# Optimization experiments

Measured on AMD Instinct MI355X. Metric: run time of the kernel, lower is better.

The kernel has to match this reference:

```python
import jax, jax.numpy as jnp
import numpy as np

B, IN, OUT, NUM_F = 131072, 128, 128, 8


def setup_inputs() -> dict:
    key = jax.random.key(0)
    ks = jax.random.split(key, 6)
    x = jax.random.normal(ks[0], (B, IN), dtype=jnp.float32)
    grid = jnp.arange(NUM_F, dtype=jnp.float32) + 1.0            # nn.Parameter(arange(num_f)+1)
    base_weight = jax.random.normal(ks[1], (OUT, IN), dtype=jnp.float32) * 0.05
    scale_sp = jnp.ones((OUT,), dtype=jnp.float32)
    coef = jax.random.uniform(ks[2], (IN, NUM_F), dtype=jnp.float32)  # torch.rand
    # Conv1d(in=IN*NUM_F, out=OUT*NUM_F, k=1, groups=NUM_F) == per-frequency [OUT, IN] matmul
    fan_in = IN  # per-group in-channels * kernel_size(1)
    bound = 1.0 / np.sqrt(fan_in)
    conv_w = jax.random.uniform(ks[3], (NUM_F, OUT, IN), dtype=jnp.float32,
                                minval=-bound, maxval=bound)
    conv_b = jax.random.uniform(ks[4], (NUM_F, OUT), dtype=jnp.float32,
                                minval=-bound, maxval=bound)
    return {"x": x, "grid": grid, "base_weight": base_weight,
            "scale_sp": scale_sp, "coef": coef, "conv_w": conv_w, "conv_b": conv_b}


def reference(x, grid, base_weight, scale_sp, coef, conv_w, conv_b):
    # base path: SiLU(x) @ W_base^T  -> [B, OUT]
    base_out = jax.nn.silu(x) @ base_weight.T
    # Fourier basis: sin(grid_f * x_i) -> [B, F, I]
    s = jnp.sin(x[:, None, :] * grid[None, :, None])
    # coef [I, F] broadcast-multiplied per (i, f)
    s = s * coef.T[None, :, :]                      # [B, F, I]
    # grouped 1x1 conv == per-frequency matmul, plus per-(f, o) bias
    spline = jnp.einsum('bfi,foi->bfo', s, conv_w) + conv_b[None, :, :]  # [B, F, OUT]
    spline_out = spline.sum(axis=1) * scale_sp      # [B, OUT]
    return base_out + spline_out
```

## Files before the change

### kernel.cpp

```cpp
#include <hip/hip_runtime.h>
#include <stdint.h>

#define NCHUNK 9
#define IN_DIM 128
#define OUT_DIM 128
#define NUM_F 8
#define B_TOTAL 131072

#define WBASE_ELEMS (OUT_DIM * IN_DIM)
#define WSIN_ELEMS (8 * OUT_DIM * IN_DIM)
#define SG_SLICE 32768

typedef __bf16 bf16x8 __attribute__((ext_vector_type(8)));
typedef float floatx16 __attribute__((ext_vector_type(16)));

typedef __attribute__((address_space(1))) const unsigned int gas_u32;
typedef __attribute__((address_space(3))) unsigned int las_u32;

__device__ __forceinline__ unsigned short f2bf_rn(float f) {
  unsigned u = __builtin_bit_cast(unsigned, f);
  u += 0x7FFFu + ((u >> 16) & 1u);
  return (unsigned short)(u >> 16);
}

__global__ void skan_prep(const float* __restrict__ base_w,
                          const float* __restrict__ scale_sp,
                          const float* __restrict__ coef,
                          const float* __restrict__ conv_w,
                          const float* __restrict__ conv_b,
                          unsigned short* __restrict__ Wbase,
                          unsigned short* __restrict__ Wsin,
                          float* __restrict__ bias) {
  int b = blockIdx.x;
  int i = threadIdx.x;
  int j = i & 7, q2 = (i >> 3) & 1;
  if (b < NCHUNK * OUT_DIM) {
    int c = b >> 7;
    int o = b & 127;
    if (c == 0) {
      float v = base_w[o * IN_DIM + i];
      int s = i >> 4;
      Wbase[(s * 2 + q2) * 1024 + o * 8 + j] = f2bf_rn(v);
    } else {
      int f = c - 1;
      float v = conv_w[(f * OUT_DIM + o) * IN_DIM + i] * coef[i * NUM_F + f] * scale_sp[o];
      int sg = i >> 5, s2 = (i >> 4) & 1;
      Wsin[((sg * 8 + f) * 4 + s2 * 2 + q2) * 1024 + o * 8 + j] = f2bf_rn(v);
    }
  } else {
    float s = 0.f;
#pragma unroll
    for (int f = 0; f < NUM_F; ++f) s += conv_b[f * OUT_DIM + i];
    bias[i] = s * scale_sp[i];
  }
}

__device__ __forceinline__ unsigned pack2(float lo, float hi) {
  unsigned ulo = __builtin_bit_cast(unsigned, lo) + 0x8000u;
  unsigned uhi = __builtin_bit_cast(unsigned, hi) + 0x8000u;
  return __builtin_amdgcn_perm(uhi, ulo, 0x07060302u);
}

__device__ __forceinline__ bf16x8 pack_frag(const float* v) {
  union { unsigned u[4]; bf16x8 f; } r;
  r.u[0] = pack2(v[0], v[1]);
  r.u[1] = pack2(v[2], v[3]);
  r.u[2] = pack2(v[4], v[5]);
  r.u[3] = pack2(v[6], v[7]);
  return r.f;
}

__device__ __forceinline__ float silu(float v) {
  return v * __builtin_amdgcn_rcpf(1.f + __expf(-v));
}

__global__ __launch_bounds__(256, 2)
void skan_main(const float* __restrict__ x,
               const unsigned short* __restrict__ Wbase,
               const unsigned short* __restrict__ Wsin,
               const float* __restrict__ bias,
               float* __restrict__ out) {
  __shared__ unsigned short sB[SG_SLICE];

  const int tid  = threadIdx.x;
  const int lane = tid & 63;
  const int w    = tid >> 6;
  const int m    = lane & 31;
  const int q2   = lane >> 5;
  const int rowBase = blockIdx.x * 256 + w * 64;

  const int fragCol = m * 8;

  floatx16 acc[2][4];
#pragma unroll
  for (int mt = 0; mt < 2; ++mt)
#pragma unroll
    for (int nt = 0; nt < 4; ++nt)
#pragma unroll
      for (int e = 0; e < 16; ++e) acc[mt][nt][e] = 0.f;

  const float* xr0 = x + (size_t)(rowBase + m) * IN_DIM;
  const float* xr1 = xr0 + 32 * IN_DIM;

#pragma unroll 1
  for (int sg = 0; sg < 4; ++sg) {
    {
      const char* src = (const char*)(Wsin + sg * SG_SLICE);
      char* dst = (char*)sB;
      int off = tid * 16;
#pragma unroll
      for (int it = 0; it < 16; ++it) {
        __builtin_amdgcn_global_load_lds((gas_u32*)(src + off), (las_u32*)(dst + off),
                                         16, 0, 0);
        off += 4096;
      }
    }

    float xv[2][2][8];
#pragma unroll
    for (int mt = 0; mt < 2; ++mt) {
      const float* xr = mt ? xr1 : xr0;
#pragma unroll
      for (int s2 = 0; s2 < 2; ++s2) {
        float4 a = *(const float4*)(xr + sg * 32 + s2 * 16 + q2 * 8);
        float4 b = *(const float4*)(xr + sg * 32 + s2 * 16 + q2 * 8 + 4);
        xv[mt][s2][0] = a.x; xv[mt][s2][1] = a.y;
        xv[mt][s2][2] = a.z; xv[mt][s2][3] = a.w;
        xv[mt][s2][4] = b.x; xv[mt][s2][5] = b.y;
        xv[mt][s2][6] = b.z; xv[mt][s2][7] = b.w;
      }
    }

#pragma unroll
    for (int s2 = 0; s2 < 2; ++s2) {
      int4 Bb[4];
#pragma unroll
      for (int nt = 0; nt < 4; ++nt)
        Bb[nt] = *(const int4*)(Wbase + ((sg * 2 + s2) * 2 + q2) * 1024 +
                                nt * 256 + fragCol);
      float sv[16];
#pragma unroll
      for (int mt = 0; mt < 2; ++mt)
#pragma unroll
        for (int j = 0; j < 8; ++j) sv[mt * 8 + j] = silu(xv[mt][s2][j]);
      bf16x8 a0 = pack_frag(&sv[0]);
      bf16x8 a1 = pack_frag(&sv[8]);
#pragma unroll
      for (int nt = 0; nt < 4; ++nt) {
        bf16x8 bf = __builtin_bit_cast(bf16x8, Bb[nt]);
        acc[0][nt] = __builtin_amdgcn_mfma_f32_32x32x16_bf16(a0, bf, acc[0][nt], 0, 0, 0);
        acc[1][nt] = __builtin_amdgcn_mfma_f32_32x32x16_bf16(a1, bf, acc[1][nt], 0, 0, 0);
      }
    }

    __syncthreads();

#pragma unroll
    for (int s2 = 0; s2 < 2; ++s2) {
      float sp[16], spp[16], c2[16];
#pragma unroll
      for (int mt = 0; mt < 2; ++mt)
#pragma unroll
        for (int j = 0; j < 8; ++j) {
          int v = mt * 8 + j;
          float xx = xv[mt][s2][j];
          sp[v]  = __sinf(xx);
          c2[v]  = 2.f * __cosf(xx);
          spp[v] = 0.f;
        }

#pragma unroll
      for (int c = 1; c <= 8; ++c) {
        bf16x8 Bf[4];
        const unsigned short* bp = sB + ((c - 1) * 4 + s2 * 2 + q2) * 1024 + fragCol;
#pragma unroll
        for (int nt = 0; nt < 4; ++nt)
          Bf[nt] = *(const bf16x8*)(bp + nt * 256);

        if (c >= 2) {
#pragma unroll
          for (int v = 0; v < 16; ++v) {
            float t = __builtin_fmaf(c2[v], sp[v], -spp[v]);
            spp[v] = sp[v];
            sp[v] = t;
          }
        }
        bf16x8 a0 = pack_frag(&sp[0]);
        bf16x8 a1 = pack_frag(&sp[8]);
#pragma unroll
        for (int nt = 0; nt < 4; ++nt) {
          acc[0][nt] = __builtin_amdgcn_mfma_f32_32x32x16_bf16(a0, Bf[nt], acc[0][nt], 0, 0, 0);
          acc[1][nt] = __builtin_amdgcn_mfma_f32_32x32x16_bf16(a1, Bf[nt], acc[1][nt], 0, 0, 0);
        }
      }
    }

    __syncthreads();
  }

#pragma unroll
  for (int mt = 0; mt < 2; ++mt) {
    float* obase = out + (size_t)(rowBase + mt * 32) * OUT_DIM + m;
#pragma unroll
    for (int nt = 0; nt < 4; ++nt) {
      float bv = bias[nt * 32 + m];
#pragma unroll
      for (int e = 0; e < 16; ++e) {
        int rl = (e & 3) + 8 * (e >> 2) + 4 * q2;
        obase[(size_t)rl * OUT_DIM + nt * 32] = acc[mt][nt][e] + bv;
      }
    }
  }
}

extern "C" void kernel_launch(void* const* d_in, const int* in_sizes, int n_in,
                              void* d_out, int out_size, void* d_ws, size_t ws_size,
                              hipStream_t stream) {
  const float* x      = (const float*)d_in[0];
  const float* base_w = (const float*)d_in[2];
  const float* scale  = (const float*)d_in[3];
  const float* coef   = (const float*)d_in[4];
  const float* conv_w = (const float*)d_in[5];
  const float* conv_b = (const float*)d_in[6];

  unsigned short* Wbase = (unsigned short*)d_ws;
  unsigned short* Wsin  = Wbase + WBASE_ELEMS;
  float* bias = (float*)(Wsin + WSIN_ELEMS);
  float* out  = (float*)d_out;

  skan_prep<<<NCHUNK * OUT_DIM + 1, 128, 0, stream>>>(base_w, scale, coef,
                                                      conv_w, conv_b, Wbase, Wsin, bias);
  skan_main<<<B_TOTAL / 256, 256, 0, stream>>>(x, Wbase, Wsin, bias, out);
}
```

Baseline: 150.4 us.

## Drop LDS staging of sin weights and halve per-wave row tile

Removes the shared-memory staging of the Fourier weight slice and its barriers. Each wave now reads B fragments straight from global memory, relying on L2/L1 caching. Each wave handles 32 rows instead of 64, the grid doubles, and launch bounds rise to 3 blocks per SIMD to improve occupancy. Each weight fragment is now reused across half as many rows, so global/L2 traffic for weights roughly doubles per output row.

```diff
diff --git a/kernel.cpp b/kernel.cpp
--- a/kernel.cpp
+++ b/kernel.cpp
@@ -13,9 +13,6 @@
 
 typedef __bf16 bf16x8 __attribute__((ext_vector_type(8)));
 typedef float floatx16 __attribute__((ext_vector_type(16)));
-
-typedef __attribute__((address_space(1))) const unsigned int gas_u32;
-typedef __attribute__((address_space(3))) unsigned int las_u32;
 
 __device__ __forceinline__ unsigned short f2bf_rn(float f) {
   unsigned u = __builtin_bit_cast(unsigned, f);
@@ -74,61 +71,40 @@
   return v * __builtin_amdgcn_rcpf(1.f + __expf(-v));
 }
 
-__global__ __launch_bounds__(256, 2)
+__global__ __launch_bounds__(256, 3)
 void skan_main(const float* __restrict__ x,
                const unsigned short* __restrict__ Wbase,
                const unsigned short* __restrict__ Wsin,
                const float* __restrict__ bias,
                float* __restrict__ out) {
-  __shared__ unsigned short sB[SG_SLICE];
-
   const int tid  = threadIdx.x;
   const int lane = tid & 63;
   const int w    = tid >> 6;
   const int m    = lane & 31;
   const int q2   = lane >> 5;
-  const int rowBase = blockIdx.x * 256 + w * 64;
+  const int rowBase = blockIdx.x * 128 + w * 32;
 
   const int fragCol = m * 8;
 
-  floatx16 acc[2][4];
+  floatx16 acc[4];
 #pragma unroll
-  for (int mt = 0; mt < 2; ++mt)
+  for (int nt = 0; nt < 4; ++nt)
 #pragma unroll
-    for (int nt = 0; nt < 4; ++nt)
-#pragma unroll
-      for (int e = 0; e < 16; ++e) acc[mt][nt][e] = 0.f;
+    for (int e = 0; e < 16; ++e) acc[nt][e] = 0.f;
 
-  const float* xr0 = x + (size_t)(rowBase + m) * IN_DIM;
-  const float* xr1 = xr0 + 32 * IN_DIM;
+  const float* xr = x + (size_t)(rowBase + m) * IN_DIM;
 
 #pragma unroll 1
   for (int sg = 0; sg < 4; ++sg) {
-    {
-      const char* src = (const char*)(Wsin + sg * SG_SLICE);
-      char* dst = (char*)sB;
-      int off = tid * 16;
+    float xv[2][8];
 #pragma unroll
-      for (int it = 0; it < 16; ++it) {
-        __builtin_amdgcn_global_load_lds((gas_u32*)(src + off), (las_u32*)(dst + off),
-                                         16, 0, 0);
-        off += 4096;
-      }
-    }
-
-    float xv[2][2][8];
-#pragma unroll
-    for (int mt = 0; mt < 2; ++mt) {
-      const float* xr = mt ? xr1 : xr0;
-#pragma unroll
-      for (int s2 = 0; s2 < 2; ++s2) {
-        float4 a = *(const float4*)(xr + sg * 32 + s2 * 16 + q2 * 8);
-        float4 b = *(const float4*)(xr + sg * 32 + s2 * 16 + q2 * 8 + 4);
-        xv[mt][s2][0] = a.x; xv[mt][s2][1] = a.y;
-        xv[mt][s2][2] = a.z; xv[mt][s2][3] = a.w;
-        xv[mt][s2][4] = b.x; xv[mt][s2][5] = b.y;
-        xv[mt][s2][6] = b.z; xv[mt][s2][7] = b.w;
-      }
+    for (int s2 = 0; s2 < 2; ++s2) {
+      float4 a = *(const float4*)(xr + sg * 32 + s2 * 16 + q2 * 8);
+      float4 b = *(const float4*)(xr + sg * 32 + s2 * 16 + q2 * 8 + 4);
+      xv[s2][0] = a.x; xv[s2][1] = a.y;
+      xv[s2][2] = a.z; xv[s2][3] = a.w;
+      xv[s2][4] = b.x; xv[s2][5] = b.y;
+      xv[s2][6] = b.z; xv[s2][7] = b.w;
     }
 
 #pragma unroll
@@ -138,77 +114,61 @@
       for (int nt = 0; nt < 4; ++nt)
         Bb[nt] = *(const int4*)(Wbase + ((sg * 2 + s2) * 2 + q2) * 1024 +
                                 nt * 256 + fragCol);
-      float sv[16];
+      float sv[8];
 #pragma unroll
-      for (int mt = 0; mt < 2; ++mt)
-#pragma unroll
-        for (int j = 0; j < 8; ++j) sv[mt * 8 + j] = silu(xv[mt][s2][j]);
-      bf16x8 a0 = pack_frag(&sv[0]);
-      bf16x8 a1 = pack_frag(&sv[8]);
+      for (int j = 0; j < 8; ++j) sv[j] = silu(xv[s2][j]);
+      bf16x8 a0 = pack_frag(sv);
 #pragma unroll
       for (int nt = 0; nt < 4; ++nt) {
         bf16x8 bf = __builtin_bit_cast(bf16x8, Bb[nt]);
-        acc[0][nt] = __builtin_amdgcn_mfma_f32_32x32x16_bf16(a0, bf, acc[0][nt], 0, 0, 0);
-        acc[1][nt] = __builtin_amdgcn_mfma_f32_32x32x16_bf16(a1, bf, acc[1][nt], 0, 0, 0);
+        acc[nt] = __builtin_amdgcn_mfma_f32_32x32x16_bf16(a0, bf, acc[nt], 0, 0, 0);
       }
     }
 
-    __syncthreads();
-
+    const unsigned short* wsg = Wsin + sg * SG_SLICE;
 #pragma unroll
     for (int s2 = 0; s2 < 2; ++s2) {
-      float sp[16], spp[16], c2[16];
+      float sp[8], spp[8], c2[8];
 #pragma unroll
-      for (int mt = 0; mt < 2; ++mt)
-#pragma unroll
-        for (int j = 0; j < 8; ++j) {
-          int v = mt * 8 + j;
-          float xx = xv[mt][s2][j];
-          sp[v]  = __sinf(xx);
-          c2[v]  = 2.f * __cosf(xx);
-          spp[v] = 0.f;
-        }
+      for (int j = 0; j < 8; ++j) {
+        float xx = xv[s2][j];
+        sp[j]  = __sinf(xx);
+        c2[j]  = 2.f * __cosf(xx);
+        spp[j] = 0.f;
+      }
 
 #pragma unroll
       for (int c = 1; c <= 8; ++c) {
         bf16x8 Bf[4];
-        const unsigned short* bp = sB + ((c - 1) * 4 + s2 * 2 + q2) * 1024 + fragCol;
+        const unsigned short* bp = wsg + ((c - 1) * 4 + s2 * 2 + q2) * 1024 + fragCol;
 #pragma unroll
         for (int nt = 0; nt < 4; ++nt)
           Bf[nt] = *(const bf16x8*)(bp + nt * 256);
 
         if (c >= 2) {
 #pragma unroll
-          for (int v = 0; v < 16; ++v) {
-            float t = __builtin_fmaf(c2[v], sp[v], -spp[v]);
-            spp[v] = sp[v];
-            sp[v] = t;
+          for (int j = 0; j < 8; ++j) {
+            float t = __builtin_fmaf(c2[j], sp[j], -spp[j]);
+            spp[j] = sp[j];
+            sp[j] = t;
           }
         }
-        bf16x8 a0 = pack_frag(&sp[0]);
-        bf16x8 a1 = pack_frag(&sp[8]);
+        bf16x8 a0 = pack_frag(sp);
 #pragma unroll
-        for (int nt = 0; nt < 4; ++nt) {
-          acc[0][nt] = __builtin_amdgcn_mfma_f32_32x32x16_bf16(a0, Bf[nt], acc[0][nt], 0, 0, 0);
-          acc[1][nt] = __builtin_amdgcn_mfma_f32_32x32x16_bf16(a1, Bf[nt], acc[1][nt], 0, 0, 0);
-        }
+        for (int nt = 0; nt < 4; ++nt)
+          acc[nt] = __builtin_amdgcn_mfma_f32_32x32x16_bf16(a0, Bf[nt], acc[nt], 0, 0, 0);
       }
     }
-
-    __syncthreads();
   }
 
+  float* obase = out + (size_t)rowBase * OUT_DIM + m;
 #pragma unroll
-  for (int mt = 0; mt < 2; ++mt) {
-    float* obase = out + (size_t)(rowBase + mt * 32) * OUT_DIM + m;
+  for (int nt = 0; nt < 4; ++nt) {
+    float bv = bias[nt * 32 + m];
 #pragma unroll
-    for (int nt = 0; nt < 4; ++nt) {
-      float bv = bias[nt * 32 + m];
-#pragma unroll
-      for (int e = 0; e < 16; ++e) {
-        int rl = (e & 3) + 8 * (e >> 2) + 4 * q2;
-        obase[(size_t)rl * OUT_DIM + nt * 32] = acc[mt][nt][e] + bv;
-      }
+    for (int e = 0; e < 16; ++e) {
+      int rl = (e & 3) + 8 * (e >> 2) + 4 * q2;
+      obase[(size_t)rl * OUT_DIM + nt * 32] = acc[nt][e] + bv;
     }
   }
 }
@@ -230,5 +190,5 @@
 
   skan_prep<<<NCHUNK * OUT_DIM + 1, 128, 0, stream>>>(base_w, scale, coef,
                                                       conv_w, conv_b, Wbase, Wsin, bias);
-  skan_main<<<B_TOTAL / 256, 256, 0, stream>>>(x, Wbase, Wsin, bias, out);
+  skan_main<<<B_TOTAL / 128, 256, 0, stream>>>(x, Wbase, Wsin, bias, out);
 }
```

Measured after the change: 224.7 us. +49.4%, slower.

## Switch to fp16 MFMA, split output columns across warps, halve tile rows

Applied to the files above, without the earlier changes.

Precision moves from bf16 to fp16, using the hardware packed convert (cvt_pkrtz) in place of manual bf16 packing. Each block now handles 128 rows instead of 256, with the four warps arranged 2x2 so each computes 64 rows by 64 output columns. The K loop now runs 8 stages of 16 inputs instead of 4 of 32, so the LDS slice shrinks to 32 KB and the launch bound targets 3 blocks per CU. The intent is higher occupancy and more CUs busy. The cost is that every x tile is loaded and every sine basis computed twice (once per column warp), plus more barriers per block.

```diff
diff --git a/kernel.cpp b/kernel.cpp
--- a/kernel.cpp
+++ b/kernel.cpp
@@ -9,18 +9,17 @@
 
 #define WBASE_ELEMS (OUT_DIM * IN_DIM)
 #define WSIN_ELEMS (8 * OUT_DIM * IN_DIM)
-#define SG_SLICE 32768
-
-typedef __bf16 bf16x8 __attribute__((ext_vector_type(8)));
+#define SLICE 16384
+
+typedef _Float16 hf16x8 __attribute__((ext_vector_type(8)));
 typedef float floatx16 __attribute__((ext_vector_type(16)));
 
 typedef __attribute__((address_space(1))) const unsigned int gas_u32;
 typedef __attribute__((address_space(3))) unsigned int las_u32;
 
-__device__ __forceinline__ unsigned short f2bf_rn(float f) {
-  unsigned u = __builtin_bit_cast(unsigned, f);
-  u += 0x7FFFu + ((u >> 16) & 1u);
-  return (unsigned short)(u >> 16);
+__device__ __forceinline__ unsigned short f2h_rn(float f) {
+  _Float16 h = (_Float16)f;
+  return __builtin_bit_cast(unsigned short, h);
 }
 
 __global__ void skan_prep(const float* __restrict__ base_w,
@@ -39,13 +38,11 @@
     int o = b & 127;
     if (c == 0) {
       float v = base_w[o * IN_DIM + i];
-      int s = i >> 4;
-      Wbase[(s * 2 + q2) * 1024 + o * 8 + j] = f2bf_rn(v);
+      Wbase[((i >> 4) * 2 + q2) * 1024 + o * 8 + j] = f2h_rn(v);
     } else {
       int f = c - 1;
       float v = conv_w[(f * OUT_DIM + o) * IN_DIM + i] * coef[i * NUM_F + f] * scale_sp[o];
-      int sg = i >> 5, s2 = (i >> 4) & 1;
-      Wsin[((sg * 8 + f) * 4 + s2 * 2 + q2) * 1024 + o * 8 + j] = f2bf_rn(v);
+      Wsin[((i >> 4) * 16 + f * 2 + q2) * 1024 + o * 8 + j] = f2h_rn(v);
     }
   } else {
     float s = 0.f;
@@ -55,18 +52,12 @@
   }
 }
 
-__device__ __forceinline__ unsigned pack2(float lo, float hi) {
-  unsigned ulo = __builtin_bit_cast(unsigned, lo) + 0x8000u;
-  unsigned uhi = __builtin_bit_cast(unsigned, hi) + 0x8000u;
-  return __builtin_amdgcn_perm(uhi, ulo, 0x07060302u);
-}
-
-__device__ __forceinline__ bf16x8 pack_frag(const float* v) {
-  union { unsigned u[4]; bf16x8 f; } r;
-  r.u[0] = pack2(v[0], v[1]);
-  r.u[1] = pack2(v[2], v[3]);
-  r.u[2] = pack2(v[4], v[5]);
-  r.u[3] = pack2(v[6], v[7]);
+__device__ __forceinline__ hf16x8 hpack(const float* v) {
+  union { unsigned u[4]; hf16x8 f; } r;
+  r.u[0] = __builtin_bit_cast(unsigned, __builtin_amdgcn_cvt_pkrtz(v[0], v[1]));
+  r.u[1] = __builtin_bit_cast(unsigned, __builtin_amdgcn_cvt_pkrtz(v[2], v[3]));
+  r.u[2] = __builtin_bit_cast(unsigned, __builtin_amdgcn_cvt_pkrtz(v[4], v[5]));
+  r.u[3] = __builtin_bit_cast(unsigned, __builtin_amdgcn_cvt_pkrtz(v[6], v[7]));
   return r.f;
 }
 
@@ -74,28 +65,30 @@
   return v * __builtin_amdgcn_rcpf(1.f + __expf(-v));
 }
 
-__global__ __launch_bounds__(256, 2)
+__global__ __launch_bounds__(256, 3)
 void skan_main(const float* __restrict__ x,
                const unsigned short* __restrict__ Wbase,
                const unsigned short* __restrict__ Wsin,
                const float* __restrict__ bias,
                float* __restrict__ out) {
-  __shared__ unsigned short sB[SG_SLICE];
+  __shared__ unsigned short sB[SLICE];
 
   const int tid  = threadIdx.x;
   const int lane = tid & 63;
   const int w    = tid >> 6;
+  const int wr   = w >> 1;
+  const int wc   = w & 1;
   const int m    = lane & 31;
   const int q2   = lane >> 5;
-  const int rowBase = blockIdx.x * 256 + w * 64;
-
-  const int fragCol = m * 8;
-
-  floatx16 acc[2][4];
+  const int rowBase = blockIdx.x * 128 + wr * 64;
+
+  const int colOff = wc * 512 + m * 8;
+
+  floatx16 acc[2][2];
 #pragma unroll
   for (int mt = 0; mt < 2; ++mt)
 #pragma unroll
-    for (int nt = 0; nt < 4; ++nt)
+    for (int nt = 0; nt < 2; ++nt)
 #pragma unroll
       for (int e = 0; e < 16; ++e) acc[mt][nt][e] = 0.f;
 
@@ -103,67 +96,59 @@
   const float* xr1 = xr0 + 32 * IN_DIM;
 
 #pragma unroll 1
-  for (int sg = 0; sg < 4; ++sg) {
+  for (int p = 0; p < 8; ++p) {
     {
-      const char* src = (const char*)(Wsin + sg * SG_SLICE);
+      const char* src = (const char*)(Wsin + p * SLICE);
       char* dst = (char*)sB;
       int off = tid * 16;
 #pragma unroll
-      for (int it = 0; it < 16; ++it) {
+      for (int it = 0; it < 8; ++it) {
         __builtin_amdgcn_global_load_lds((gas_u32*)(src + off), (las_u32*)(dst + off),
                                          16, 0, 0);
         off += 4096;
       }
     }
 
-    float xv[2][2][8];
+    float xv[2][8];
 #pragma unroll
     for (int mt = 0; mt < 2; ++mt) {
       const float* xr = mt ? xr1 : xr0;
-#pragma unroll
-      for (int s2 = 0; s2 < 2; ++s2) {
-        float4 a = *(const float4*)(xr + sg * 32 + s2 * 16 + q2 * 8);
-        float4 b = *(const float4*)(xr + sg * 32 + s2 * 16 + q2 * 8 + 4);
-        xv[mt][s2][0] = a.x; xv[mt][s2][1] = a.y;
-        xv[mt][s2][2] = a.z; xv[mt][s2][3] = a.w;
-        xv[mt][s2][4] = b.x; xv[mt][s2][5] = b.y;
-        xv[mt][s2][6] = b.z; xv[mt][s2][7] = b.w;
-      }
-    }
-
-#pragma unroll
-    for (int s2 = 0; s2 < 2; ++s2) {
-      int4 Bb[4];
-#pragma unroll
-      for (int nt = 0; nt < 4; ++nt)
-        Bb[nt] = *(const int4*)(Wbase + ((sg * 2 + s2) * 2 + q2) * 1024 +
-                                nt * 256 + fragCol);
+      float4 a = *(const float4*)(xr + p * 16 + q2 * 8);
+      float4 b = *(const float4*)(xr + p * 16 + q2 * 8 + 4);
+      xv[mt][0] = a.x; xv[mt][1] = a.y; xv[mt][2] = a.z; xv[mt][3] = a.w;
+      xv[mt][4] = b.x; xv[mt][5] = b.y; xv[mt][6] = b.z; xv[mt][7] = b.w;
+    }
+
+    {
+      int4 Bb[2];
+#pragma unroll
+      for (int nt = 0; nt < 2; ++nt)
+        Bb[nt] = *(const int4*)(Wbase + (p * 2 + q2) * 1024 + colOff + nt * 256);
       float sv[16];
 #pragma unroll
       for (int mt = 0; mt < 2; ++mt)
 #pragma unroll
-        for (int j = 0; j < 8; ++j) sv[mt * 8 + j] = silu(xv[mt][s2][j]);
-      bf16x8 a0 = pack_frag(&sv[0]);
-      bf16x8 a1 = pack_frag(&sv[8]);
-#pragma unroll
-      for (int nt = 0; nt < 4; ++nt) {
-        bf16x8 bf = __builtin_bit_cast(bf16x8, Bb[nt]);
-        acc[0][nt] = __builtin_amdgcn_mfma_f32_32x32x16_bf16(a0, bf, acc[0][nt], 0, 0, 0);
-        acc[1][nt] = __builtin_amdgcn_mfma_f32_32x32x16_bf16(a1, bf, acc[1][nt], 0, 0, 0);
+        for (int j = 0; j < 8; ++j) sv[mt * 8 + j] = silu(xv[mt][j]);
+      hf16x8 a0 = hpack(&sv[0]);
+      hf16x8 a1 = hpack(&sv[8]);
+#pragma unroll
+      for (int nt = 0; nt < 2; ++nt) {
+        hf16x8 bf = __builtin_bit_cast(hf16x8, Bb[nt]);
+        acc[0][nt] = __builtin_amdgcn_mfma_f32_32x32x16_f16(a0, bf, acc[0][nt], 0, 0, 0);
+        acc[1][nt] = __builtin_amdgcn_mfma_f32_32x32x16_f16(a1, bf, acc[1][nt], 0, 0, 0);
       }
     }
 
     __syncthreads();
 
-#pragma unroll
-    for (int s2 = 0; s2 < 2; ++s2) {
+    {
       float sp[16], spp[16], c2[16];
 #pragma unroll
       for (int mt = 0; mt < 2; ++mt)
 #pragma unroll
         for (int j = 0; j < 8; ++j) {
           int v = mt * 8 + j;
-          float xx = xv[mt][s2][j];
+          float xx = xv[mt][j];
           sp[v]  = __sinf(xx);
           c2[v]  = 2.f * __cosf(xx);
           spp[v] = 0.f;
@@ -171,11 +156,11 @@
 
 #pragma unroll
       for (int c = 1; c <= 8; ++c) {
-        bf16x8 Bf[4];
-        const unsigned short* bp = sB + ((c - 1) * 4 + s2 * 2 + q2) * 1024 + fragCol;
-#pragma unroll
-        for (int nt = 0; nt < 4; ++nt)
-          Bf[nt] = *(const bf16x8*)(bp + nt * 256);
+        hf16x8 Bf[2];
+        const unsigned short* bp = sB + ((c - 1) * 2 + q2) * 1024 + colOff;
+#pragma unroll
+        for (int nt = 0; nt < 2; ++nt)
+          Bf[nt] = *(const hf16x8*)(bp + nt * 256);
 
         if (c >= 2) {
 #pragma unroll
@@ -185,12 +170,12 @@
             sp[v] = t;
           }
         }
-        bf16x8 a0 = pack_frag(&sp[0]);
-        bf16x8 a1 = pack_frag(&sp[8]);
-#pragma unroll
-        for (int nt = 0; nt < 4; ++nt) {
-          acc[0][nt] = __builtin_amdgcn_mfma_f32_32x32x16_bf16(a0, Bf[nt], acc[0][nt], 0, 0, 0);
-          acc[1][nt] = __builtin_amdgcn_mfma_f32_32x32x16_bf16(a1, Bf[nt], acc[1][nt], 0, 0, 0);
+        hf16x8 a0 = hpack(&sp[0]);
+        hf16x8 a1 = hpack(&sp[8]);
+#pragma unroll
+        for (int nt = 0; nt < 2; ++nt) {
+          acc[0][nt] = __builtin_amdgcn_mfma_f32_32x32x16_f16(a0, Bf[nt], acc[0][nt], 0, 0, 0);
+          acc[1][nt] = __builtin_amdgcn_mfma_f32_32x32x16_f16(a1, Bf[nt], acc[1][nt], 0, 0, 0);
         }
       }
     }
@@ -200,10 +185,10 @@
 
 #pragma unroll
   for (int mt = 0; mt < 2; ++mt) {
-    float* obase = out + (size_t)(rowBase + mt * 32) * OUT_DIM + m;
-#pragma unroll
-    for (int nt = 0; nt < 4; ++nt) {
-      float bv = bias[nt * 32 + m];
+    float* obase = out + (size_t)(rowBase + mt * 32) * OUT_DIM + wc * 64 + m;
+#pragma unroll
+    for (int nt = 0; nt < 2; ++nt) {
+      float bv = bias[wc * 64 + nt * 32 + m];
 #pragma unroll
       for (int e = 0; e < 16; ++e) {
         int rl = (e & 3) + 8 * (e >> 2) + 4 * q2;
@@ -230,5 +215,5 @@
 
   skan_prep<<<NCHUNK * OUT_DIM + 1, 128, 0, stream>>>(base_w, scale, coef,
                                                       conv_w, conv_b, Wbase, Wsin, bias);
-  skan_main<<<B_TOTAL / 256, 256, 0, stream>>>(x, Wbase, Wsin, bias, out);
-}
+  skan_main<<<B_TOTAL / 128, 256, 0, stream>>>(x, Wbase, Wsin, bias, out);
+}
```

Measured after the change: 160.7 us. +6.8%, slower.
